# Optimization experiments

Measured on AMD Instinct MI355X. Metric: run time of the kernel, lower is better.

## Reference

```python
import jax, jax.numpy as jnp
import numpy as np

B, QL, D = 4, 1024, 1024
H, HD = 16, 64
KVL = 2048


def setup_inputs() -> dict:
    key = jax.random.key(0)
    ks = jax.random.split(key, 6)
    scale = 1.0 / np.sqrt(D)
    return {
        "hidden_states": jax.random.normal(ks[0], (B, QL, D), dtype=jnp.float32),
        "key_states": jax.random.normal(ks[1], (B, H, KVL, HD), dtype=jnp.float32),
        "value_states": jax.random.normal(ks[2], (B, H, KVL, HD), dtype=jnp.float32),
        "attention_mask": jnp.zeros((B, 1, 1, KVL), dtype=jnp.float32),
        "Wq": jax.random.normal(ks[3], (D, D), dtype=jnp.float32) * scale,
        "Wo": jax.random.normal(ks[4], (D, D), dtype=jnp.float32) * scale,
    }


def reference(hidden_states, key_states, value_states, attention_mask, Wq, Wo):
    batch = hidden_states.shape[0]
    # Q projection (T5 Linear has no bias), split heads: [B, H, Q, HD]
    q = jnp.einsum("bqd,de->bqe", hidden_states, Wq)
    q = q.reshape(batch, -1, H, HD).transpose(0, 2, 1, 3)
    # NOTE: T5 attention has NO 1/sqrt(d) scaling
    scores = jnp.einsum("bhqd,bhkd->bhqk", q, key_states) + attention_mask
    attn = jax.nn.softmax(scores.astype(jnp.float32), axis=-1).astype(scores.dtype)
    out = jnp.einsum("bhqk,bhkd->bhqd", attn, value_states)
    out = out.transpose(0, 2, 1, 3).reshape(batch, -1, H * HD)
    return jnp.einsum("bqe,ed->bqd", out, Wo)
```

## Files before the change

kernel.cpp:

```cpp
#include <hip/hip_runtime.h>
#include <hip/hip_bf16.h>
#include <hip/hip_fp16.h>
#include <stdint.h>

typedef _Float16 f16;
typedef _Float16 f16x2 __attribute__((ext_vector_type(2)));
typedef _Float16 f16x4 __attribute__((ext_vector_type(4)));
typedef _Float16 f16x8 __attribute__((ext_vector_type(8)));
typedef float f32x4 __attribute__((ext_vector_type(4)));
typedef float f32x16 __attribute__((ext_vector_type(16)));

#define B_ 4
#define QL_ 1024
#define D_ 1024
#define H_ 16
#define HD_ 64
#define KVL_ 2048
#define L2E 1.44269504088896f

__device__ __forceinline__ void g2lds16(const void* g, void* l) {
    __builtin_amdgcn_global_load_lds(
        (const __attribute__((address_space(1))) uint32_t*)g,
        (__attribute__((address_space(3))) uint32_t*)l,
        16, 0, 0);
}

union U8 { uint32_t u[4]; f16x8 v; };

__device__ __forceinline__ uint32_t pkrtz(float a, float b) {
    auto t = __builtin_amdgcn_cvt_pkrtz(a, b);
    return __builtin_bit_cast(uint32_t, t);
}

__global__ void preprocess(const float* __restrict__ hs, f16* __restrict__ hs_h,
                           const float* __restrict__ K, f16* __restrict__ K_h,
                           const float* __restrict__ Wq, f16* __restrict__ Wq_t,
                           const float* __restrict__ Wo, f16* __restrict__ Wo_t,
                           const float* __restrict__ V, f16* __restrict__ V_t,
                           const float* __restrict__ mask, float* __restrict__ mL) {
    __shared__ float t[64][65];
    int bid = blockIdx.x, tid = threadIdx.x;
    if (bid < 1024) {
        const int n4 = (B_ * QL_ * D_) / 4;
        for (int i = bid * 256 + tid; i < n4; i += 1024 * 256) {
            float4 v = ((const float4*)hs)[i];
            f16x4 o = { (f16)v.x, (f16)v.y, (f16)v.z, (f16)v.w };
            ((f16x4*)hs_h)[i] = o;
        }
    } else if (bid < 3072) {
        int t0 = (bid - 1024) * 256 + tid;
#pragma unroll
        for (int rep = 0; rep < 2; ++rep) {
            int U = t0 + rep * 524288;
            int bh = U >> 14, rem = U & 16383;
            int ch = rem >> 9, r2 = rem & 511;
            int dsl = r2 >> 7, r3 = r2 & 127;
            int kv = r3 >> 1, hi2 = r3 & 1;
            const float* sp = K + (((size_t)bh * KVL_ + ch * 64 + kv) * HD_ + dsl * 16 + hi2 * 8);
            f16x8 o;
#pragma unroll
            for (int j = 0; j < 8; ++j) o[j] = (f16)sp[j];
            *(f16x8*)(K_h + (size_t)U * 8) = o;
        }
    } else if (bid < 3584) {
        int wbid = bid - 3072;
        const float* src = wbid < 256 ? Wq : Wo;
        f16* dst = wbid < 256 ? Wq_t : Wo_t;
        int b2 = wbid & 255;
        int k0 = (b2 >> 4) << 6, n0 = (b2 & 15) << 6;
        int rr = tid >> 4, c4 = (tid & 15) << 2;
#pragma unroll
        for (int i = 0; i < 4; ++i) {
            int r = i * 16 + rr;
            float4 v = *(const float4*)(src + (size_t)(k0 + r) * 1024 + n0 + c4);
            t[r][c4 + 0] = v.x; t[r][c4 + 1] = v.y; t[r][c4 + 2] = v.z; t[r][c4 + 3] = v.w;
        }
        __syncthreads();
#pragma unroll
        for (int i = 0; i < 4; ++i) {
            int n = i * 16 + rr;
            f16x4 o;
#pragma unroll
            for (int j = 0; j < 4; ++j) o[j] = (f16)t[c4 + j][n];
            *(f16x4*)(dst + (size_t)(n0 + n) * 1024 + k0 + c4) = o;
        }
    } else if (bid < 5632) {
        int vb = bid - 3584;
        int bh = vb >> 5, ch = vb & 31;
        int rr = tid >> 4, c4 = (tid & 15) << 2;
#pragma unroll
        for (int i = 0; i < 4; ++i) {
            int r = i * 16 + rr;
            float4 v = *(const float4*)(V + ((size_t)bh * KVL_ + ch * 64 + r) * HD_ + c4);
            t[r][c4 + 0] = v.x; t[r][c4 + 1] = v.y; t[r][c4 + 2] = v.z; t[r][c4 + 3] = v.w;
        }
        __syncthreads();
#pragma unroll
        for (int rep = 0; rep < 2; ++rep) {
            int u = tid + rep * 256;
            int st = u >> 7, d = (u >> 1) & 63, hi2 = u & 1;
            f16x8 o;
#pragma unroll
            for (int j = 0; j < 8; ++j) {
                int kvl = st * 16 + (j & 3) + 8 * (j >> 2) + 4 * hi2;
                o[j] = (f16)t[kvl][d];
            }
            *(f16x8*)(V_t + ((size_t)(bh * 32 + ch) * 512 + u) * 8) = o;
        }
    } else {
        int i = (bid - 5632) * 256 + tid;
        if (i < (B_ * KVL_) / 4) {
            f32x4 v = ((const f32x4*)mask)[i];
            v *= L2E;
            ((f32x4*)mL)[i] = v;
        }
    }
}

template <int EPI>
__global__ __launch_bounds__(512) void gemm_tn(
    const f16* __restrict__ A, const f16* __restrict__ BT, void* __restrict__ Cout,
    int M, int N, int K) {
    __shared__ char Alds[2][16384];
    __shared__ char Blds[2][8192];
    int d0 = blockIdx.x;
    int xcd = d0 & 7, sx = d0 >> 3;
    int bm = xcd * 4 + (sx & 3);
    int bn = sx >> 2;
    int tid = threadIdx.x, w = tid >> 6, l = tid & 63;
    int l15 = l & 15, lg = l >> 4;
    int wm = w >> 1, wn = w & 1;
    f32x4 acc[2][2] = {};

    const char* ag0; const char* ag1; int ao0, ao1;
    {
        int i0 = w, i1 = w + 8;
        int r0 = i0 * 8 + (l >> 3), r1 = i1 * 8 + (l >> 3);
        int c0 = (l & 7) ^ (r0 & 7), c1 = (l & 7) ^ (r1 & 7);
        ag0 = (const char*)A + ((size_t)(bm * 128 + r0) * K + c0 * 8) * 2;
        ag1 = (const char*)A + ((size_t)(bm * 128 + r1) * K + c1 * 8) * 2;
        ao0 = i0 * 1024; ao1 = i1 * 1024;
    }
    int rB = w * 8 + (l >> 3);
    int ccB = (l & 7) ^ (rB & 7);
    const char* bgp = (const char*)BT + ((size_t)(bn * 64 + rB) * K + ccB * 8) * 2;
    int boB = w * 1024;

    int aoff[2][2], boff[2][2];
#pragma unroll
    for (int ks = 0; ks < 2; ++ks)
#pragma unroll
        for (int m = 0; m < 2; ++m) {
            int ra = wm * 32 + m * 16 + l15;
            aoff[ks][m] = ra * 128 + ((ks * 64 + lg * 16) ^ ((ra & 7) << 4));
            int rb = wn * 32 + m * 16 + l15;
            boff[ks][m] = rb * 128 + ((ks * 64 + lg * 16) ^ ((rb & 7) << 4));
        }
    const char* Ab = &Alds[0][0];
    const char* Bb = &Blds[0][0];

#define GSTAGE(buf, soff)                                      \
    {                                                          \
        g2lds16(ag0 + (soff), &Alds[buf][ao0]);                \
        g2lds16(ag1 + (soff), &Alds[buf][ao1]);                \
        g2lds16(bgp + (soff), &Blds[buf][boB]);                \
    }
#define GCOMP(buf)                                                               \
    _Pragma("unroll") for (int ks = 0; ks < 2; ++ks) {                           \
        f16x8 af[2], bf[2];                                                      \
        af[0] = *(const f16x8*)(Ab + (buf) * 16384 + aoff[ks][0]);               \
        af[1] = *(const f16x8*)(Ab + (buf) * 16384 + aoff[ks][1]);               \
        bf[0] = *(const f16x8*)(Bb + (buf) * 8192 + boff[ks][0]);                \
        bf[1] = *(const f16x8*)(Bb + (buf) * 8192 + boff[ks][1]);                \
        _Pragma("unroll") for (int m = 0; m < 2; ++m)                            \
            _Pragma("unroll") for (int n = 0; n < 2; ++n)                        \
                acc[m][n] = __builtin_amdgcn_mfma_f32_16x16x32_f16(af[m], bf[n], acc[m][n], 0, 0, 0); \
    }

    GSTAGE(0, 0);
    asm volatile("s_waitcnt vmcnt(0)" ::: "memory");
    __syncthreads();

    for (int t2 = 0; t2 < 8; ++t2) {
        GSTAGE(1, 128);
        GCOMP(0);
        asm volatile("s_waitcnt vmcnt(0)" ::: "memory");
        __syncthreads();
        if (t2 < 7) GSTAGE(0, 256);
        GCOMP(1);
        asm volatile("s_waitcnt vmcnt(0)" ::: "memory");
        __syncthreads();
        ag0 += 256; ag1 += 256; bgp += 256;
    }

#pragma unroll
    for (int m = 0; m < 2; ++m)
#pragma unroll
        for (int n = 0; n < 2; ++n)
#pragma unroll
            for (int i = 0; i < 4; ++i) {
                int row = bm * 128 + wm * 32 + m * 16 + lg * 4 + i;
                int col = bn * 64 + wn * 32 + n * 16 + l15;
                if (EPI == 0) {
                    float v = acc[m][n][i] * L2E;
                    int b = row >> 10, q = row & 1023, h = col >> 6, d = col & 63;
                    ((f16*)Cout)[(((size_t)b * H_ + h) * QL_ + q) * HD_ + d] = (f16)v;
                } else {
                    ((float*)Cout)[(size_t)row * N + col] = acc[m][n][i];
                }
            }
#undef GSTAGE
#undef GCOMP
}

__global__ __launch_bounds__(512, 4) void attn_fused(
    const f16* __restrict__ qh, const f16* __restrict__ kh, const f16* __restrict__ vt,
    const float* __restrict__ mL, f16* __restrict__ aout) {
    __shared__ char lds_buf[65536];
    __shared__ float msk[2][1024];
    __shared__ float frl[8][32];
    __shared__ float fr2[4][2][32];
    __shared__ float2 msx[4][32];

    int tid = threadIdx.x, w = tid >> 6, l = tid & 63;
    int l31 = l & 31, hi = l >> 5;
    int g = w >> 2, wg = w & 3;
    int d0 = blockIdx.x;
    int xcd = d0 & 7, sx = d0 >> 3;
    int bh = xcd * 8 + (sx & 7);
    int qt = sx >> 3;
    int b = bh >> 4, h = bh & 15;

    const char* lbase = lds_buf + g * 32768 + l31 * 32 + hi * 16;
    const char* mlb = (const char*)&msk[g][0] + hi * 16;

    f16x8 Qf[4];
    {
        const f16* qp = qh + ((size_t)bh * QL_ + qt * 128 + wg * 32 + l31) * HD_ + hi * 8;
#pragma unroll
        for (int ds_ = 0; ds_ < 4; ++ds_) Qf[ds_] = *(const f16x8*)(qp + ds_ * 16);
    }

    int i0 = wg * 2;
    const char* kgp0 = (const char*)kh + (((size_t)(bh * 32 + g * 16) * 512) + i0 * 64 + l) * 16;
    const char* kgp1 = kgp0 + 1024;
    const char* vgp0 = (const char*)vt + (((size_t)(bh * 32 + g * 16) * 512) + i0 * 64 + l) * 16;
    const char* vgp1 = vgp0 + 1024;
    char* kl0 = lds_buf + g * 32768 + i0 * 1024;
    char* kl1 = kl0 + 1024;
    char* vl0 = lds_buf + g * 32768 + 16384 + i0 * 1024;
    char* vl1 = vl0 + 1024;

#define PREF(buf, soff)                                  \
    {                                                    \
        g2lds16(kgp0 + (soff), kl0 + (buf) * 8192);      \
        g2lds16(kgp1 + (soff), kl1 + (buf) * 8192);      \
        g2lds16(vgp0 + (soff), vl0 + (buf) * 8192);      \
        g2lds16(vgp1 + (soff), vl1 + (buf) * 8192);      \
    }

    float mrun = -1e30f, ssA = 0.f, ssB = 0.f;
    f32x16 acc[2] = {};
    const f16x2 one2 = { (f16)1.0f, (f16)1.0f };

#define BODY(buf, kb, mo)                                                                 \
    {                                                                                     \
        f32x16 St;                                                                        \
        _Pragma("unroll") for (int g4 = 0; g4 < 4; ++g4) {                                \
            f32x4 mv = *(const f32x4*)(mlb + (mo) + (kb) * 128 + g4 * 32);                \
            St[g4 * 4 + 0] = mv[0]; St[g4 * 4 + 1] = mv[1];                               \
            St[g4 * 4 + 2] = mv[2]; St[g4 * 4 + 3] = mv[3];                               \
        }                                                                                 \
        __builtin_amdgcn_s_setprio(1);                                                    \
        _Pragma("unroll") for (int ds_ = 0; ds_ < 4; ++ds_) {                             \
            f16x8 kf = *(const f16x8*)(lbase + (buf) * 8192 + ds_ * 2048 + (kb) * 1024);  \
            St = __builtin_amdgcn_mfma_f32_32x32x16_f16(kf, Qf[ds_], St, 0, 0, 0);        \
        }                                                                                 \
        __builtin_amdgcn_s_setprio(0);                                                    \
        float a0 = fmaxf(fmaxf(St[0], St[1]), St[2]);                                     \
        float a1 = fmaxf(fmaxf(St[3], St[4]), St[5]);                                     \
        float a2 = fmaxf(fmaxf(St[6], St[7]), St[8]);                                     \
        float a3 = fmaxf(fmaxf(St[9], St[10]), St[11]);                                   \
        float a4 = fmaxf(fmaxf(St[12], St[13]), St[14]);                                  \
        float lmax = fmaxf(fmaxf(fmaxf(a0, a1), St[15]), fmaxf(a2, fmaxf(a3, a4)));       \
        if (__any(lmax > mrun + 12.f)) {                                                  \
            float pm = fmaxf(lmax, __shfl_xor(lmax, 32));                                 \
            float mn = fmaxf(mrun, pm);                                                   \
            float fac = __builtin_amdgcn_exp2f(mrun - mn);                                \
            mrun = mn; ssA *= fac; ssB *= fac;                                            \
            frl[w][l31] = fac;                                                            \
            asm volatile("s_waitcnt lgkmcnt(0)" ::: "memory");                            \
            _Pragma("unroll") for (int g4 = 0; g4 < 4; ++g4) {                            \
                f32x4 fv = *(const f32x4*)&frl[w][g4 * 8 + hi * 4];                       \
                _Pragma("unroll") for (int c = 0; c < 2; ++c)                             \
                    _Pragma("unroll") for (int j = 0; j < 4; ++j)                         \
                        acc[c][g4 * 4 + j] *= fv[j];                                      \
            }                                                                             \
        }                                                                                 \
        uint32_t pk[8];                                                                   \
        _Pragma("unroll") for (int i = 0; i < 8; ++i) {                                   \
            float p0 = __builtin_amdgcn_exp2f(St[2 * i] - mrun);                          \
            float p1 = __builtin_amdgcn_exp2f(St[2 * i + 1] - mrun);                      \
            pk[i] = pkrtz(p0, p1);                                                        \
        }                                                                                 \
        _Pragma("unroll") for (int i = 0; i < 4; ++i) {                                   \
            ssA = __builtin_amdgcn_fdot2(__builtin_bit_cast(f16x2, pk[2 * i]), one2, ssA, false);     \
            ssB = __builtin_amdgcn_fdot2(__builtin_bit_cast(f16x2, pk[2 * i + 1]), one2, ssB, false); \
        }                                                                                 \
        __builtin_amdgcn_s_setprio(1);                                                    \
        _Pragma("unroll") for (int sti = 0; sti < 2; ++sti) {                             \
            U8 pa;                                                                        \
            pa.u[0] = pk[sti * 4 + 0]; pa.u[1] = pk[sti * 4 + 1];                         \
            pa.u[2] = pk[sti * 4 + 2]; pa.u[3] = pk[sti * 4 + 3];                         \
            const int st_ = (kb) * 2 + sti;                                               \
            _Pragma("unroll") for (int c = 0; c < 2; ++c) {                               \
                U8 vb;                                                                    \
                vb.v = *(const f16x8*)(lbase + 16384 + (buf) * 8192 + st_ * 2048 + c * 1024); \
                acc[c] = __builtin_amdgcn_mfma_f32_32x32x16_f16(pa.v, vb.v, acc[c], 0, 0, 0); \
            }                                                                             \
        }                                                                                 \
        __builtin_amdgcn_s_setprio(0);                                                    \
    }

    g2lds16((const char*)(mL + b * KVL_ + g * 1024 + wg * 256), (char*)&msk[g][wg * 256]);
    PREF(0, 0);
    asm volatile("s_waitcnt vmcnt(0)" ::: "memory");
    __syncthreads();

    for (int it = 0; it < 8; ++it) {
        PREF(1, 8192);
        BODY(0, 0, 0);
        BODY(0, 1, 0);
        asm volatile("s_waitcnt vmcnt(0)" ::: "memory");
        __syncthreads();
        if (it < 7) PREF(0, 16384);
        BODY(1, 0, 256);
        BODY(1, 1, 256);
        asm volatile("s_waitcnt vmcnt(0)" ::: "memory");
        __syncthreads();
        kgp0 += 16384; kgp1 += 16384; vgp0 += 16384; vgp1 += 16384;
        mlb += 512;
    }

    float ssum = ssA + ssB;
    ssum += __shfl_xor(ssum, 32);
    char* exch = lds_buf;
    if (g == 1) {
        int base = (wg * 64 + l) * 128;
#pragma unroll
        for (int i = 0; i < 8; ++i) {
            int c = i >> 2, j0 = (i & 3) * 4;
            f32x4 vv = { acc[c][j0], acc[c][j0 + 1], acc[c][j0 + 2], acc[c][j0 + 3] };
            *(f32x4*)(exch + base + ((i * 16) ^ ((l & 7) << 4))) = vv;
        }
        if (hi == 0) msx[wg][l31] = make_float2(mrun, ssum);
    }
    __syncthreads();
    if (g == 0) {
        float2 mb = msx[wg][l31];
        float m = fmaxf(mrun, mb.x);
        float fA = __builtin_amdgcn_exp2f(mrun - m);
        float fB = __builtin_amdgcn_exp2f(mb.x - m);
        float s = ssum * fA + mb.y * fB;
        float rinv = 1.0f / s;
        if (hi == 0) { fr2[wg][0][l31] = fA * rinv; fr2[wg][1][l31] = fB * rinv; }
        asm volatile("s_waitcnt lgkmcnt(0)" ::: "memory");
        int base = (wg * 64 + l) * 128;
#pragma unroll
        for (int c = 0; c < 2; ++c)
#pragma unroll
            for (int g4 = 0; g4 < 4; ++g4) {
                f32x4 gAv = *(const f32x4*)&fr2[wg][0][g4 * 8 + hi * 4];
                f32x4 gBv = *(const f32x4*)&fr2[wg][1][g4 * 8 + hi * 4];
                int i = c * 4 + g4;
                f32x4 pv = *(const f32x4*)(exch + base + ((i * 16) ^ ((l & 7) << 4)));
#pragma unroll
                for (int j = 0; j < 4; ++j) {
                    float o = acc[c][g4 * 4 + j] * gAv[j] + pv[j] * gBv[j];
                    int q = qt * 128 + wg * 32 + g4 * 8 + hi * 4 + j;
                    int dd = c * 32 + l31;
                    aout[((size_t)b * QL_ + q) * D_ + h * HD_ + dd] = (f16)o;
                }
            }
    }
#undef PREF
#undef BODY
}

extern "C" void kernel_launch(void* const* d_in, const int* in_sizes, int n_in,
                              void* d_out, int out_size, void* d_ws, size_t ws_size,
                              hipStream_t stream) {
    const float* hs = (const float*)d_in[0];
    const float* K  = (const float*)d_in[1];
    const float* V  = (const float*)d_in[2];
    const float* mask = (const float*)d_in[3];
    const float* Wq = (const float*)d_in[4];
    const float* Wo = (const float*)d_in[5];
    float* out = (float*)d_out;
    char* ws = (char*)d_ws;

    f16* hs_h = (f16*)(ws + 0);
    f16* Wq_t = (f16*)(ws + 8388608);
    f16* Wo_t = (f16*)(ws + 10485760);
    f16* K_h  = (f16*)(ws + 12582912);
    f16* V_t  = (f16*)(ws + 29360128);
    f16* q_h  = (f16*)(ws + 46137344);
    f16* a_o  = (f16*)(ws + 54525952);
    float* mL = (float*)(ws + 62914560);

    preprocess<<<5640, 256, 0, stream>>>(hs, hs_h, K, K_h, Wq, Wq_t, Wo, Wo_t,
                                         V, V_t, mask, mL);
    gemm_tn<0><<<512, 512, 0, stream>>>(hs_h, Wq_t, (void*)q_h, 4096, 1024, 1024);
    attn_fused<<<512, 512, 0, stream>>>(q_h, K_h, V_t, mL, a_o);
    gemm_tn<1><<<512, 512, 0, stream>>>(a_o, Wo_t, (void*)out, 4096, 1024, 1024);
}
```

Baseline: 107.1 us.

## Overlap K/V/Wo/mask conversion with Q-projection GEMM in one launch

The preprocess kernel now converts only hidden states and Wq. The K, V, Wo and mask conversion work moves into extra blocks of the Q-projection GEMM launch, so it runs alongside the GEMM instead of serially before it. Separately, the attention kernel drops its LDS staging of the mask and reads mask values directly from global memory in each body step. The trade-offs are more block-scheduling imbalance and larger shared-memory use in the combined launch, plus extra global loads per attention iteration.

```diff
diff --git a/kernel.cpp b/kernel.cpp
--- a/kernel.cpp
+++ b/kernel.cpp
@@ -32,12 +32,8 @@
     return __builtin_bit_cast(uint32_t, t);
 }
 
-__global__ void preprocess(const float* __restrict__ hs, f16* __restrict__ hs_h,
-                           const float* __restrict__ K, f16* __restrict__ K_h,
-                           const float* __restrict__ Wq, f16* __restrict__ Wq_t,
-                           const float* __restrict__ Wo, f16* __restrict__ Wo_t,
-                           const float* __restrict__ V, f16* __restrict__ V_t,
-                           const float* __restrict__ mask, float* __restrict__ mL) {
+__global__ void preprocess_slim(const float* __restrict__ hs, f16* __restrict__ hs_h,
+                                const float* __restrict__ Wq, f16* __restrict__ Wq_t) {
     __shared__ float t[64][65];
     int bid = blockIdx.x, tid = threadIdx.x;
     if (bid < 1024) {
@@ -47,8 +43,121 @@
             f16x4 o = { (f16)v.x, (f16)v.y, (f16)v.z, (f16)v.w };
             ((f16x4*)hs_h)[i] = o;
         }
-    } else if (bid < 3072) {
-        int t0 = (bid - 1024) * 256 + tid;
+    } else {
+        int b2 = bid - 1024;
+        int k0 = (b2 >> 4) << 6, n0 = (b2 & 15) << 6;
+        int rr = tid >> 4, c4 = (tid & 15) << 2;
+#pragma unroll
+        for (int i = 0; i < 4; ++i) {
+            int r = i * 16 + rr;
+            float4 v = *(const float4*)(Wq + (size_t)(k0 + r) * 1024 + n0 + c4);
+            t[r][c4 + 0] = v.x; t[r][c4 + 1] = v.y; t[r][c4 + 2] = v.z; t[r][c4 + 3] = v.w;
+        }
+        __syncthreads();
+#pragma unroll
+        for (int i = 0; i < 4; ++i) {
+            int n = i * 16 + rr;
+            f16x4 o;
+#pragma unroll
+            for (int j = 0; j < 4; ++j) o[j] = (f16)t[c4 + j][n];
+            *(f16x4*)(Wq_t + (size_t)(n0 + n) * 1024 + k0 + c4) = o;
+        }
+    }
+}
+
+__global__ __launch_bounds__(512) void gemm0_fused(
+    const f16* __restrict__ A, const f16* __restrict__ BT, f16* __restrict__ q_h,
+    const float* __restrict__ K, f16* __restrict__ K_h,
+    const float* __restrict__ V, f16* __restrict__ V_t,
+    const float* __restrict__ Wo, f16* __restrict__ Wo_t,
+    const float* __restrict__ mask, float* __restrict__ mL) {
+    __shared__ char shmem[49152];
+    int bid = blockIdx.x, tid = threadIdx.x;
+
+    if (bid < 512) {
+        char* Alds = shmem;
+        char* Blds = shmem + 32768;
+        int xcd = bid & 7, sx = bid >> 3;
+        int bm = xcd * 4 + (sx & 3);
+        int bn = sx >> 2;
+        int w = tid >> 6, l = tid & 63;
+        int l15 = l & 15, lg = l >> 4;
+        int wm = w >> 1, wn = w & 1;
+        f32x4 acc[2][2] = {};
+
+        const char* ag0; const char* ag1; int ao0, ao1;
+        {
+            int i0 = w, i1 = w + 8;
+            int r0 = i0 * 8 + (l >> 3), r1 = i1 * 8 + (l >> 3);
+            int c0 = (l & 7) ^ (r0 & 7), c1 = (l & 7) ^ (r1 & 7);
+            ag0 = (const char*)A + ((size_t)(bm * 128 + r0) * 1024 + c0 * 8) * 2;
+            ag1 = (const char*)A + ((size_t)(bm * 128 + r1) * 1024 + c1 * 8) * 2;
+            ao0 = i0 * 1024; ao1 = i1 * 1024;
+        }
+        int rB = w * 8 + (l >> 3);
+        int ccB = (l & 7) ^ (rB & 7);
+        const char* bgp = (const char*)BT + ((size_t)(bn * 64 + rB) * 1024 + ccB * 8) * 2;
+        int boB = w * 1024;
+
+        int aoff[2][2], boff[2][2];
+#pragma unroll
+        for (int ks = 0; ks < 2; ++ks)
+#pragma unroll
+            for (int m = 0; m < 2; ++m) {
+                int ra = wm * 32 + m * 16 + l15;
+                aoff[ks][m] = ra * 128 + ((ks * 64 + lg * 16) ^ ((ra & 7) << 4));
+                int rb = wn * 32 + m * 16 + l15;
+                boff[ks][m] = rb * 128 + ((ks * 64 + lg * 16) ^ ((rb & 7) << 4));
+            }
+
+#define GSTAGE(buf, soff)                                          \
+    {                                                              \
+        g2lds16(ag0 + (soff), Alds + (buf) * 16384 + ao0);         \
+        g2lds16(ag1 + (soff), Alds + (buf) * 16384 + ao1);         \
+        g2lds16(bgp + (soff), Blds + (buf) * 8192 + boB);          \
+    }
+#define GCOMP(buf)                                                               \
+    _Pragma("unroll") for (int ks = 0; ks < 2; ++ks) {                           \
+        f16x8 af[2], bf[2];                                                      \
+        af[0] = *(const f16x8*)(Alds + (buf) * 16384 + aoff[ks][0]);             \
+        af[1] = *(const f16x8*)(Alds + (buf) * 16384 + aoff[ks][1]);             \
+        bf[0] = *(const f16x8*)(Blds + (buf) * 8192 + boff[ks][0]);              \
+        bf[1] = *(const f16x8*)(Blds + (buf) * 8192 + boff[ks][1]);              \
+        _Pragma("unroll") for (int m = 0; m < 2; ++m)                            \
+            _Pragma("unroll") for (int n = 0; n < 2; ++n)                        \
+                acc[m][n] = __builtin_amdgcn_mfma_f32_16x16x32_f16(af[m], bf[n], acc[m][n], 0, 0, 0); \
+    }
+
+        GSTAGE(0, 0);
+        asm volatile("s_waitcnt vmcnt(0)" ::: "memory");
+        __syncthreads();
+        for (int t2 = 0; t2 < 8; ++t2) {
+            GSTAGE(1, 128);
+            GCOMP(0);
+            asm volatile("s_waitcnt vmcnt(0)" ::: "memory");
+            __syncthreads();
+            if (t2 < 7) GSTAGE(0, 256);
+            GCOMP(1);
+            asm volatile("s_waitcnt vmcnt(0)" ::: "memory");
+            __syncthreads();
+            ag0 += 256; ag1 += 256; bgp += 256;
+        }
+#pragma unroll
+        for (int m = 0; m < 2; ++m)
+#pragma unroll
+            for (int n = 0; n < 2; ++n)
+#pragma unroll
+                for (int i = 0; i < 4; ++i) {
+                    int row = bm * 128 + wm * 32 + m * 16 + lg * 4 + i;
+                    int col = bn * 64 + wn * 32 + n * 16 + l15;
+                    float v = acc[m][n][i] * L2E;
+                    int b = row >> 10, q = row & 1023, h = col >> 6, d = col & 63;
+                    q_h[(((size_t)b * H_ + h) * QL_ + q) * HD_ + d] = (f16)v;
+                }
+#undef GSTAGE
+#undef GCOMP
+    } else if (bid < 1536) {
+        int t0 = (bid - 512) * 512 + tid;
 #pragma unroll
         for (int rep = 0; rep < 2; ++rep) {
             int U = t0 + rep * 524288;
@@ -62,18 +171,42 @@
             for (int j = 0; j < 8; ++j) o[j] = (f16)sp[j];
             *(f16x8*)(K_h + (size_t)U * 8) = o;
         }
-    } else if (bid < 3584) {
-        int wbid = bid - 3072;
-        const float* src = wbid < 256 ? Wq : Wo;
-        f16* dst = wbid < 256 ? Wq_t : Wo_t;
-        int b2 = wbid & 255;
-        int k0 = (b2 >> 4) << 6, n0 = (b2 & 15) << 6;
-        int rr = tid >> 4, c4 = (tid & 15) << 2;
+    } else if (bid < 2560) {
+        int sub = tid >> 8, st2 = tid & 255;
+        int vb = (bid - 1536) * 2 + sub;
+        int bh = vb >> 5, ch = vb & 31;
+        float (*tt)[65] = (float(*)[65])(shmem + sub * 16640);
+        int rr = st2 >> 4, c4 = (st2 & 15) << 2;
 #pragma unroll
         for (int i = 0; i < 4; ++i) {
             int r = i * 16 + rr;
-            float4 v = *(const float4*)(src + (size_t)(k0 + r) * 1024 + n0 + c4);
-            t[r][c4 + 0] = v.x; t[r][c4 + 1] = v.y; t[r][c4 + 2] = v.z; t[r][c4 + 3] = v.w;
+            float4 v = *(const float4*)(V + ((size_t)bh * KVL_ + ch * 64 + r) * HD_ + c4);
+            tt[r][c4 + 0] = v.x; tt[r][c4 + 1] = v.y; tt[r][c4 + 2] = v.z; tt[r][c4 + 3] = v.w;
+        }
+        __syncthreads();
+#pragma unroll
+        for (int rep = 0; rep < 2; ++rep) {
+            int u = st2 + rep * 256;
+            int st = u >> 7, d = (u >> 1) & 63, hi2 = u & 1;
+            f16x8 o;
+#pragma unroll
+            for (int j = 0; j < 8; ++j) {
+                int kvl = st * 16 + (j & 3) + 8 * (j >> 2) + 4 * hi2;
+                o[j] = (f16)tt[kvl][d];
+            }
+            *(f16x8*)(V_t + ((size_t)(bh * 32 + ch) * 512 + u) * 8) = o;
+        }
+    } else if (bid < 2688) {
+        int sub = tid >> 8, st2 = tid & 255;
+        int b2 = (bid - 2560) * 2 + sub;
+        float (*tt)[65] = (float(*)[65])(shmem + sub * 16640);
+        int k0 = (b2 >> 4) << 6, n0 = (b2 & 15) << 6;
+        int rr = st2 >> 4, c4 = (st2 & 15) << 2;
+#pragma unroll
+        for (int i = 0; i < 4; ++i) {
+            int r = i * 16 + rr;
+            float4 v = *(const float4*)(Wo + (size_t)(k0 + r) * 1024 + n0 + c4);
+            tt[r][c4 + 0] = v.x; tt[r][c4 + 1] = v.y; tt[r][c4 + 2] = v.z; tt[r][c4 + 3] = v.w;
         }
         __syncthreads();
 #pragma unroll
@@ -81,34 +214,11 @@
             int n = i * 16 + rr;
             f16x4 o;
 #pragma unroll
-            for (int j = 0; j < 4; ++j) o[j] = (f16)t[c4 + j][n];
-            *(f16x4*)(dst + (size_t)(n0 + n) * 1024 + k0 + c4) = o;
-        }
-    } else if (bid < 5632) {
-        int vb = bid - 3584;
-        int bh = vb >> 5, ch = vb & 31;
-        int rr = tid >> 4, c4 = (tid & 15) << 2;
-#pragma unroll
-        for (int i = 0; i < 4; ++i) {
-            int r = i * 16 + rr;
-            float4 v = *(const float4*)(V + ((size_t)bh * KVL_ + ch * 64 + r) * HD_ + c4);
-            t[r][c4 + 0] = v.x; t[r][c4 + 1] = v.y; t[r][c4 + 2] = v.z; t[r][c4 + 3] = v.w;
-        }
-        __syncthreads();
-#pragma unroll
-        for (int rep = 0; rep < 2; ++rep) {
-            int u = tid + rep * 256;
-            int st = u >> 7, d = (u >> 1) & 63, hi2 = u & 1;
-            f16x8 o;
-#pragma unroll
-            for (int j = 0; j < 8; ++j) {
-                int kvl = st * 16 + (j & 3) + 8 * (j >> 2) + 4 * hi2;
-                o[j] = (f16)t[kvl][d];
-            }
-            *(f16x8*)(V_t + ((size_t)(bh * 32 + ch) * 512 + u) * 8) = o;
+            for (int j = 0; j < 4; ++j) o[j] = (f16)tt[c4 + j][n];
+            *(f16x4*)(Wo_t + (size_t)(n0 + n) * 1024 + k0 + c4) = o;
         }
     } else {
-        int i = (bid - 5632) * 256 + tid;
+        int i = (bid - 2688) * 512 + tid;
         if (i < (B_ * KVL_) / 4) {
             f32x4 v = ((const f32x4*)mask)[i];
             v *= L2E;
@@ -117,10 +227,8 @@
     }
 }
 
-template <int EPI>
-__global__ __launch_bounds__(512) void gemm_tn(
-    const f16* __restrict__ A, const f16* __restrict__ BT, void* __restrict__ Cout,
-    int M, int N, int K) {
+__global__ __launch_bounds__(512) void gemm_tn1(
+    const f16* __restrict__ A, const f16* __restrict__ BT, float* __restrict__ Cout) {
     __shared__ char Alds[2][16384];
     __shared__ char Blds[2][8192];
     int d0 = blockIdx.x;
@@ -137,13 +245,13 @@
         int i0 = w, i1 = w + 8;
         int r0 = i0 * 8 + (l >> 3), r1 = i1 * 8 + (l >> 3);
         int c0 = (l & 7) ^ (r0 & 7), c1 = (l & 7) ^ (r1 & 7);
-        ag0 = (const char*)A + ((size_t)(bm * 128 + r0) * K + c0 * 8) * 2;
-        ag1 = (const char*)A + ((size_t)(bm * 128 + r1) * K + c1 * 8) * 2;
+        ag0 = (const char*)A + ((size_t)(bm * 128 + r0) * 1024 + c0 * 8) * 2;
+        ag1 = (const char*)A + ((size_t)(bm * 128 + r1) * 1024 + c1 * 8) * 2;
         ao0 = i0 * 1024; ao1 = i1 * 1024;
     }
     int rB = w * 8 + (l >> 3);
     int ccB = (l & 7) ^ (rB & 7);
-    const char* bgp = (const char*)BT + ((size_t)(bn * 64 + rB) * K + ccB * 8) * 2;
+    const char* bgp = (const char*)BT + ((size_t)(bn * 64 + rB) * 1024 + ccB * 8) * 2;
     int boB = w * 1024;
 
     int aoff[2][2], boff[2][2];
@@ -180,7 +288,6 @@
     GSTAGE(0, 0);
     asm volatile("s_waitcnt vmcnt(0)" ::: "memory");
     __syncthreads();
-
     for (int t2 = 0; t2 < 8; ++t2) {
         GSTAGE(1, 128);
         GCOMP(0);
@@ -192,7 +299,6 @@
         __syncthreads();
         ag0 += 256; ag1 += 256; bgp += 256;
     }
-
 #pragma unroll
     for (int m = 0; m < 2; ++m)
 #pragma unroll
@@ -201,13 +307,7 @@
             for (int i = 0; i < 4; ++i) {
                 int row = bm * 128 + wm * 32 + m * 16 + lg * 4 + i;
                 int col = bn * 64 + wn * 32 + n * 16 + l15;
-                if (EPI == 0) {
-                    float v = acc[m][n][i] * L2E;
-                    int b = row >> 10, q = row & 1023, h = col >> 6, d = col & 63;
-                    ((f16*)Cout)[(((size_t)b * H_ + h) * QL_ + q) * HD_ + d] = (f16)v;
-                } else {
-                    ((float*)Cout)[(size_t)row * N + col] = acc[m][n][i];
-                }
+                Cout[(size_t)row * 1024 + col] = acc[m][n][i];
             }
 #undef GSTAGE
 #undef GCOMP
@@ -217,7 +317,6 @@
     const f16* __restrict__ qh, const f16* __restrict__ kh, const f16* __restrict__ vt,
     const float* __restrict__ mL, f16* __restrict__ aout) {
     __shared__ char lds_buf[65536];
-    __shared__ float msk[2][1024];
     __shared__ float frl[8][32];
     __shared__ float fr2[4][2][32];
     __shared__ float2 msx[4][32];
@@ -232,7 +331,6 @@
     int b = bh >> 4, h = bh & 15;
 
     const char* lbase = lds_buf + g * 32768 + l31 * 32 + hi * 16;
-    const char* mlb = (const char*)&msk[g][0] + hi * 16;
 
     f16x8 Qf[4];
     {
@@ -261,15 +359,19 @@
 
     float mrun = -1e30f, ssA = 0.f, ssB = 0.f;
     f32x16 acc[2] = {};
+    const float* mp = mL + b * KVL_ + g * 1024 + hi * 4;
     const f16x2 one2 = { (f16)1.0f, (f16)1.0f };
 
-#define BODY(buf, kb, mo)                                                                 \
+#define BODY(buf, kb, mof)                                                                \
     {                                                                                     \
+        const float* mq = mp + (mof) + (kb) * 32;                                         \
+        f32x4 mv0 = *(const f32x4*)(mq);                                                  \
+        f32x4 mv1 = *(const f32x4*)(mq + 8);                                              \
+        f32x4 mv2 = *(const f32x4*)(mq + 16);                                             \
+        f32x4 mv3 = *(const f32x4*)(mq + 24);                                             \
         f32x16 St;                                                                        \
-        _Pragma("unroll") for (int g4 = 0; g4 < 4; ++g4) {                                \
-            f32x4 mv = *(const f32x4*)(mlb + (mo) + (kb) * 128 + g4 * 32);                \
-            St[g4 * 4 + 0] = mv[0]; St[g4 * 4 + 1] = mv[1];                               \
-            St[g4 * 4 + 2] = mv[2]; St[g4 * 4 + 3] = mv[3];                               \
+        _Pragma("unroll") for (int j = 0; j < 4; ++j) {                                   \
+            St[j] = mv0[j]; St[4 + j] = mv1[j]; St[8 + j] = mv2[j]; St[12 + j] = mv3[j];  \
         }                                                                                 \
         __builtin_amdgcn_s_setprio(1);                                                    \
         _Pragma("unroll") for (int ds_ = 0; ds_ < 4; ++ds_) {                             \
@@ -322,7 +424,6 @@
         __builtin_amdgcn_s_setprio(0);                                                    \
     }
 
-    g2lds16((const char*)(mL + b * KVL_ + g * 1024 + wg * 256), (char*)&msk[g][wg * 256]);
     PREF(0, 0);
     asm volatile("s_waitcnt vmcnt(0)" ::: "memory");
     __syncthreads();
@@ -334,12 +435,12 @@
         asm volatile("s_waitcnt vmcnt(0)" ::: "memory");
         __syncthreads();
         if (it < 7) PREF(0, 16384);
-        BODY(1, 0, 256);
-        BODY(1, 1, 256);
+        BODY(1, 0, 64);
+        BODY(1, 1, 64);
         asm volatile("s_waitcnt vmcnt(0)" ::: "memory");
         __syncthreads();
         kgp0 += 16384; kgp1 += 16384; vgp0 += 16384; vgp1 += 16384;
-        mlb += 512;
+        mp += 128;
     }
 
     float ssum = ssA + ssB;
@@ -408,9 +509,9 @@
     f16* a_o  = (f16*)(ws + 54525952);
     float* mL = (float*)(ws + 62914560);
 
-    preprocess<<<5640, 256, 0, stream>>>(hs, hs_h, K, K_h, Wq, Wq_t, Wo, Wo_t,
-                                         V, V_t, mask, mL);
-    gemm_tn<0><<<512, 512, 0, stream>>>(hs_h, Wq_t, (void*)q_h, 4096, 1024, 1024);
+    preprocess_slim<<<1280, 256, 0, stream>>>(hs, hs_h, Wq, Wq_t);
+    gemm0_fused<<<2692, 512, 0, stream>>>(hs_h, Wq_t, q_h, K, K_h, V, V_t,
+                                          Wo, Wo_t, mask, mL);
     attn_fused<<<512, 512, 0, stream>>>(q_h, K_h, V_t, mL, a_o);
-    gemm_tn<1><<<512, 512, 0, stream>>>(a_o, Wo_t, (void*)out, 4096, 1024, 1024);
-}
+    gemm_tn1<<<512, 512, 0, stream>>>(a_o, Wo_t, out);
+}
```

After: 101.6 us. 1.05x faster.
